# Kernel optimization log

Hardware: AMD Instinct MI355X
Metric: run time of the kernel (lower is better)

The kernel has to match this reference:

```python
import jax, jax.numpy as jnp
import numpy as np

B, L, D = 8, 4096, 1024
EPS = 1e-6


def setup_inputs() -> dict:
    key = jax.random.key(0)
    k1, k2, k3 = jax.random.split(key, 3)
    x = jax.random.normal(k1, (B, L, D), dtype=jnp.float32)
    # torch.nn.Linear default init ~ U(-1/sqrt(d), 1/sqrt(d)); scaled normal is fine for a reference
    w_in = jax.random.normal(k2, (3 * D, D), dtype=jnp.float32) * (D ** -0.5)
    w_out = jax.random.normal(k3, (D, D), dtype=jnp.float32) * (D ** -0.5)
    scale = jnp.ones((D,), dtype=jnp.float32)
    return {"x": x, "w_in": w_in, "w_out": w_out, "scale": scale}


def reference(x, w_in, w_out, scale):
    residual = x
    # RMSNorm: ||x||_2 * d^{-1/2}
    norm = jnp.linalg.norm(x, axis=-1, keepdims=True) * (x.shape[-1] ** -0.5)
    xn = scale * x / (norm + EPS)
    # proj_in: Linear(d, 3d, bias=False) -> chunk into g, v, f
    gvf = jnp.einsum('bld,ed->ble', xn, w_in)  # [B, L, 3D]
    g, v, f = jnp.split(gvf, 3, axis=-1)
    g = jax.nn.sigmoid(g)
    f = jax.nn.sigmoid(f - 1.0)

    # sequential gated linear recurrence: h_t = f_t * h_{t-1} + (1 - f_t) * v_t
    def step(h, fv):
        ft, vt = fv  # each [B, D]
        h = ft * h + (1.0 - ft) * vt
        return h, h

    h0 = jnp.zeros((x.shape[0], x.shape[2]), dtype=x.dtype)
    _, h_seq = jax.lax.scan(step, h0, (jnp.swapaxes(f, 0, 1), jnp.swapaxes(v, 0, 1)))
    h_seq = jnp.swapaxes(h_seq, 0, 1)  # [B, L, D]

    out = g * h_seq
    return residual + jnp.einsum('bld,ed->ble', out, w_out)
```

## Files before the change

kernel.cpp:

```cpp
#include <hip/hip_runtime.h>
#include <cstdint>
#include <cstddef>

typedef unsigned short u16;
typedef __attribute__((ext_vector_type(8))) short short8;
typedef __attribute__((ext_vector_type(4))) float floatx4;
typedef __attribute__((ext_vector_type(4))) unsigned short ushort4v;

constexpr int D_ = 1024;
constexpr int B_ = 8;
constexpr int L_ = 4096;
constexpr int M_ = B_ * L_;
constexpr int NCHUNK = 64;
constexpr int CLEN = L_ / NCHUNK;
constexpr float EPS_ = 1e-6f;
constexpr size_t WIN_ELEMS = (size_t)3 * D_ * D_;
constexpr size_t WOUT_ELEMS = (size_t)D_ * D_;
constexpr int NT_K = 16;

__device__ __forceinline__ float bf2f(u16 b) {
    union { unsigned u; float f; } x; x.u = ((unsigned)b) << 16; return x.f;
}
__device__ __forceinline__ u16 f2bf(float f) {
    union { float f; unsigned u; } x; x.f = f;
    unsigned r = x.u + 0x7fffu + ((x.u >> 16) & 1u);
    return (u16)(r >> 16);
}
__device__ __forceinline__ float sigmoidf_(float x) {
    return 1.f / (1.f + __expf(-x));
}
__device__ __forceinline__ short8 cvt8(const float* __restrict__ p) {
    float4 a = *(const float4*)p;
    float4 b = *(const float4*)(p + 4);
    short8 o;
    o[0] = (short)f2bf(a.x); o[1] = (short)f2bf(a.y);
    o[2] = (short)f2bf(a.z); o[3] = (short)f2bf(a.w);
    o[4] = (short)f2bf(b.x); o[5] = (short)f2bf(b.y);
    o[6] = (short)f2bf(b.z); o[7] = (short)f2bf(b.w);
    return o;
}
__device__ __forceinline__ void gload16(const void* g, void* l) {
    __builtin_amdgcn_global_load_lds((const __attribute__((address_space(1))) void*)g,
                                     (__attribute__((address_space(3))) void*)l, 16, 0, 0);
}

__global__ __launch_bounds__(256) void prep_xn_kernel(const float* __restrict__ x,
                                                      const float* __restrict__ scale,
                                                      u16* __restrict__ xn) {
    const int row = blockIdx.x;
    const int t = threadIdx.x;
    const float* xr = x + (size_t)row * D_;
    float4 xv = ((const float4*)xr)[t];
    float ss = xv.x * xv.x + xv.y * xv.y + xv.z * xv.z + xv.w * xv.w;
#pragma unroll
    for (int m = 32; m >= 1; m >>= 1) ss += __shfl_xor(ss, m, 64);
    __shared__ float red[4];
    const int wave = t >> 6, lane = t & 63;
    if (lane == 0) red[wave] = ss;
    __syncthreads();
    float tot = red[0] + red[1] + red[2] + red[3];
    float inv = 1.f / (sqrtf(tot * (1.f / D_)) + EPS_);
    float4 sv = ((const float4*)scale)[t];
    ushort4v o;
    o[0] = f2bf(xv.x * inv * sv.x);
    o[1] = f2bf(xv.y * inv * sv.y);
    o[2] = f2bf(xv.z * inv * sv.z);
    o[3] = f2bf(xv.w * inv * sv.w);
    ((ushort4v*)(xn + (size_t)row * D_))[t] = o;
}

__global__ __launch_bounds__(256) void prep_w_kernel(const float* __restrict__ w_in,
                                                     const float* __restrict__ w_out,
                                                     u16* __restrict__ w_in_bf,
                                                     u16* __restrict__ w_out_bf) {
    size_t i8 = ((size_t)blockIdx.x * 256 + threadIdx.x) * 8;
    if (i8 < WIN_ELEMS) {
        *(short8*)(w_in_bf + i8) = cvt8(w_in + i8);
    } else {
        size_t j = i8 - WIN_ELEMS;
        *(short8*)(w_out_bf + j) = cvt8(w_out + j);
    }
}


#define STAGE_A_(buf, half, koff) do { \
    const u16* g_ = gA0 + (koff) + (half) * 65536; \
    u16* l_ = (buf) + ((half) * 64 + iw) * 64; \
    gload16(g_, l_); gload16(g_ + 131072, l_ + 8192); } while (0)
#define STAGE_B_(buf, half, koff) do { \
    const u16* g_ = gB0 + (koff) + (half) * 32768; \
    u16* l_ = (buf) + (rBw + (half) * 32) * 64; \
    gload16(g_, l_); gload16(g_ + 131072, l_ + 8192); } while (0)
#define BARRIER_() do { __builtin_amdgcn_sched_barrier(0); \
    __builtin_amdgcn_s_barrier(); \
    __builtin_amdgcn_sched_barrier(0); } while (0)
#define LDA4_(mlo) do { \
    _Pragma("unroll") for (int m_ = 0; m_ < 4; ++m_) { \
      int o_ = aOff + ((mlo) + m_) * 2048; \
      af[m_][0] = *(const short8*)((const char*)curA + o_); \
      af[m_][1] = *(const short8*)((const char*)curA + (o_ ^ 64)); } } while (0)
#define LDB2_(nlo) do { \
    _Pragma("unroll") for (int n_ = 0; n_ < 2; ++n_) { \
      int o_ = bOff + ((nlo) + n_) * 2048; \
      bfv[n_][0] = *(const short8*)((const char*)curB + o_); \
      bfv[n_][1] = *(const short8*)((const char*)curB + (o_ ^ 64)); } } while (0)
#define MFMA_Q_(mlo, nlo) do { \
    __builtin_amdgcn_s_setprio(1); \
    _Pragma("unroll") for (int m_ = 0; m_ < 4; ++m_) \
    _Pragma("unroll") for (int n_ = 0; n_ < 2; ++n_) \
    _Pragma("unroll") for (int k_ = 0; k_ < 2; ++k_) \
      acc[(mlo) + m_][(nlo) + n_] = __builtin_amdgcn_mfma_f32_16x16x32_bf16( \
          af[m_][k_], bfv[n_][k_], acc[(mlo) + m_][(nlo) + n_], 0, 0, 0); \
    __builtin_amdgcn_s_setprio(0); } while (0)

__device__ __forceinline__ void tile_step(int tt, u16* curA, u16* curB, u16* othA, u16* othB,
                                          const u16* gA0, const u16* gB0, int iw, int rBw,
                                          int aOff, int bOff, floatx4 (&acc)[8][4]) {
    short8 af[4][2], bfv[2][2];
    const int k1 = (tt + 1) * 64, k2 = (tt + 2) * 64;
    const bool s1 = (tt + 1 < NT_K), s2 = (tt + 2 < NT_K);
    LDA4_(0); LDB2_(0);
    if (s1) STAGE_A_(othA, 1, k1);
    BARRIER_();
    MFMA_Q_(0, 0);
    BARRIER_();
    LDB2_(2);
    if (s1) STAGE_B_(othB, 1, k1);
    BARRIER_();
    MFMA_Q_(0, 2);
    BARRIER_();
    LDA4_(4); LDB2_(0);
    if (s2) STAGE_A_(curA, 0, k2);
    BARRIER_();
    MFMA_Q_(4, 0);
    BARRIER_();
    LDB2_(2);
    if (s2) STAGE_B_(curB, 0, k2);
    BARRIER_();
    MFMA_Q_(4, 2);
    if (s2)      { asm volatile("s_waitcnt vmcnt(4)" ::: "memory"); }
    else if (s1) { asm volatile("s_waitcnt vmcnt(0)" ::: "memory"); }
    BARRIER_();
}

__device__ __forceinline__ void gemm256_core(const u16* __restrict__ gA,
                                             const u16* __restrict__ gB,
                                             int m0, int n0,
                                             u16* __restrict__ As, u16* __restrict__ Bs,
                                             floatx4 (&acc)[8][4]) {
    const int t = threadIdx.x;
    const int wid = t >> 6, lane = t & 63;
    const int wr = wid >> 2, wc = wid & 3;
    const int l15 = lane & 15, quad = lane >> 4;
    const int jrow = lane >> 3, jc = lane & 7;
    const int swz = ((jc ^ (jrow & 7)) << 3);
    const u16* gA0 = gA + (size_t)(m0 + wid * 8 + jrow) * 1024 + swz;
    const int i0 = wid * 8 + jrow;
    const int rB0 = ((i0 >> 5) << 6) + (i0 & 31);
    const u16* gB0 = gB + (size_t)(n0 + rB0) * 1024 + swz;
    const int iw = wid * 8;
    const int rBw = ((iw >> 5) << 6) + (iw & 31);
    const int c0 = (quad * 16) ^ ((l15 & 7) << 4);
    const int aOff = (wr * 128 + l15) * 128 + c0;
    const int bOff = (wc * 64 + l15) * 128 + c0;

#pragma unroll
    for (int i = 0; i < 8; i++)
#pragma unroll
        for (int j = 0; j < 4; j++) { floatx4 z = {0.f, 0.f, 0.f, 0.f}; acc[i][j] = z; }

    STAGE_A_(As, 0, 0); STAGE_A_(As, 1, 0);
    STAGE_B_(Bs, 0, 0); STAGE_B_(Bs, 1, 0);
    STAGE_A_(As + 16384, 0, 64);
    STAGE_B_(Bs + 16384, 0, 64);
    asm volatile("s_waitcnt vmcnt(4)" ::: "memory");
    BARRIER_();

#pragma unroll 1
    for (int tt = 0; tt < NT_K; tt += 2) {
        tile_step(tt,     As,         Bs,         As + 16384, Bs + 16384,
                  gA0, gB0, iw, rBw, aOff, bOff, acc);
        tile_step(tt + 1, As + 16384, Bs + 16384, As,         Bs,
                  gA0, gB0, iw, rBw, aOff, bOff, acc);
    }
}

__global__ __launch_bounds__(512, 2) void gemm1_kernel(const u16* __restrict__ xn,
                                                       const u16* __restrict__ w_in,
                                                       u16* __restrict__ g_buf,
                                                       u16* __restrict__ v_buf,
                                                       u16* __restrict__ f_buf) {
    __shared__ __align__(16) u16 As[2 * 16384];
    __shared__ __align__(16) u16 Bs[2 * 16384];
    const int m0 = blockIdx.y * 256;
    const int n0 = blockIdx.x * 256;
    floatx4 acc[8][4];
    gemm256_core(xn, w_in, m0, n0, As, Bs, acc);

    const int t = threadIdx.x;
    const int wid = t >> 6, lane = t & 63;
    const int wr = wid >> 2, wc = wid & 3;
    const int l15 = lane & 15, quad = lane >> 4;
    const int plane = n0 >> 10;
    const int dcol0 = (n0 & 1023) + wc * 64;
    u16* dst = (plane == 0) ? g_buf : ((plane == 1) ? v_buf : f_buf);
    const int mrow0 = m0 + wr * 128 + quad * 4;
#pragma unroll
    for (int mt = 0; mt < 8; mt++) {
#pragma unroll
        for (int r = 0; r < 4; r++) {
            int m = mrow0 + mt * 16 + r;
#pragma unroll
            for (int nt = 0; nt < 4; nt++) {
                float val = acc[mt][nt][r];
                if (plane == 0) val = sigmoidf_(val);
                else if (plane == 2) val = sigmoidf_(val - 1.f);
                dst[(size_t)m * 1024 + dcol0 + nt * 16 + l15] = f2bf(val);
            }
        }
    }
}

__global__ __launch_bounds__(512, 2) void gemm2_kernel(const u16* __restrict__ op,
                                                       const u16* __restrict__ w_out,
                                                       const float* __restrict__ xres,
                                                       float* __restrict__ out) {
    __shared__ __align__(16) u16 As[2 * 16384];
    __shared__ __align__(16) u16 Bs[2 * 16384];
    const int m0 = blockIdx.y * 256;
    const int n0 = blockIdx.x * 256;
    floatx4 acc[8][4];
    gemm256_core(op, w_out, m0, n0, As, Bs, acc);

    const int t = threadIdx.x;
    const int wid = t >> 6, lane = t & 63;
    const int wr = wid >> 2, wc = wid & 3;
    const int l15 = lane & 15, quad = lane >> 4;
    const int ncol0 = n0 + wc * 64;
    const int mrow0 = m0 + wr * 128 + quad * 4;
#pragma unroll
    for (int mt = 0; mt < 8; mt++) {
#pragma unroll
        for (int r = 0; r < 4; r++) {
            int m = mrow0 + mt * 16 + r;
#pragma unroll
            for (int nt = 0; nt < 4; nt++) {
                size_t idx = (size_t)m * 1024 + ncol0 + nt * 16 + l15;
                out[idx] = acc[mt][nt][r] + xres[idx];
            }
        }
    }
}

__global__ __launch_bounds__(256) void scan1_kernel(const u16* __restrict__ f_buf,
                                                    const u16* __restrict__ v_buf,
                                                    float* __restrict__ Aarr,
                                                    float* __restrict__ Barr) {
    const int wid = blockIdx.x * 4 + (threadIdx.x >> 6);
    const int lane = threadIdx.x & 63;
    const int b = wid >> 10;
    const int rem = wid & 1023;
    const int c = rem >> 4;
    const int db = (rem & 15) * 64 + lane;
    float A = 1.f, Bv = 0.f;
    size_t base = ((size_t)b * L_ + c * CLEN) * D_ + db;
#pragma unroll 4
    for (int tt = 0; tt < CLEN; tt++) {
        float fv = bf2f(f_buf[base + (size_t)tt * D_]);
        float vv = bf2f(v_buf[base + (size_t)tt * D_]);
        A *= fv;
        Bv = fv * Bv + (1.f - fv) * vv;
    }
    size_t sidx = ((size_t)b * NCHUNK + c) * D_ + db;
    Aarr[sidx] = A;
    Barr[sidx] = Bv;
}

__global__ __launch_bounds__(256) void scan2_kernel(const float* __restrict__ Aarr,
                                                    const float* __restrict__ Barr,
                                                    float* __restrict__ hin) {
    const int id = blockIdx.x * 256 + threadIdx.x;
    const int b = id >> 10, d = id & 1023;
    float h = 0.f;
    for (int c = 0; c < NCHUNK; c++) {
        size_t idx = ((size_t)b * NCHUNK + c) * D_ + d;
        hin[idx] = h;
        h = Aarr[idx] * h + Barr[idx];
    }
}

__global__ __launch_bounds__(256) void scan3_kernel(const u16* __restrict__ f_buf,
                                                    const u16* __restrict__ v_buf,
                                                    u16* g_io,
                                                    const float* __restrict__ hin) {
    const int wid = blockIdx.x * 4 + (threadIdx.x >> 6);
    const int lane = threadIdx.x & 63;
    const int b = wid >> 10;
    const int rem = wid & 1023;
    const int c = rem >> 4;
    const int db = (rem & 15) * 64 + lane;
    size_t base = ((size_t)b * L_ + c * CLEN) * D_ + db;
    float h = hin[((size_t)b * NCHUNK + c) * D_ + db];
#pragma unroll 4
    for (int tt = 0; tt < CLEN; tt++) {
        size_t idx = base + (size_t)tt * D_;
        float fv = bf2f(f_buf[idx]);
        float vv = bf2f(v_buf[idx]);
        float gv = bf2f(g_io[idx]);
        h = fv * h + (1.f - fv) * vv;
        g_io[idx] = f2bf(gv * h);
    }
}

extern "C" void kernel_launch(void* const* d_in, const int* in_sizes, int n_in,
                              void* d_out, int out_size, void* d_ws, size_t ws_size,
                              hipStream_t stream) {
    const float* x     = (const float*)d_in[0];
    const float* w_in  = (const float*)d_in[1];
    const float* w_out = (const float*)d_in[2];
    const float* scale = (const float*)d_in[3];
    float* out = (float*)d_out;

    u16* f_buf = (u16*)d_out;
    u16* v_buf = (u16*)d_out + (size_t)M_ * D_;

    char* ws = (char*)d_ws;
    const size_t PLANE = (size_t)M_ * D_ * sizeof(u16);
    u16* xn    = (u16*)ws;
    u16* g_buf = (u16*)(ws + PLANE);
    u16* w_in_bf  = (u16*)(ws + 2 * PLANE);
    u16* w_out_bf = w_in_bf + WIN_ELEMS;
    float* Aarr = (float*)(ws + 2 * PLANE + (WIN_ELEMS + WOUT_ELEMS) * sizeof(u16));
    float* Barr = Aarr + (size_t)B_ * NCHUNK * D_;
    float* hin  = Barr + (size_t)B_ * NCHUNK * D_;

    prep_xn_kernel<<<M_, 256, 0, stream>>>(x, scale, xn);
    prep_w_kernel<<<(int)((WIN_ELEMS + WOUT_ELEMS) / 8 / 256), 256, 0, stream>>>(
        w_in, w_out, w_in_bf, w_out_bf);
    gemm1_kernel<<<dim3(3 * D_ / 256, M_ / 256), 512, 0, stream>>>(
        xn, w_in_bf, g_buf, v_buf, f_buf);
    scan1_kernel<<<(B_ * NCHUNK * 16) / 4, 256, 0, stream>>>(f_buf, v_buf, Aarr, Barr);
    scan2_kernel<<<(B_ * D_) / 256, 256, 0, stream>>>(Aarr, Barr, hin);
    scan3_kernel<<<(B_ * NCHUNK * 16) / 4, 256, 0, stream>>>(f_buf, v_buf, g_buf, hin);
    gemm2_kernel<<<dim3(D_ / 256, M_ / 256), 512, 0, stream>>>(g_buf, w_out_bf, x, out);
}
```

Measured before the change: 638.1 us.

## Fuse prep kernels, remap GEMM tiles per XCD, stage gemm1 epilogue through LDS

```diff
diff --git a/kernel.cpp b/kernel.cpp
--- a/kernel.cpp
+++ b/kernel.cpp
@@ -17,6 +17,7 @@
 constexpr size_t WIN_ELEMS = (size_t)3 * D_ * D_;
 constexpr size_t WOUT_ELEMS = (size_t)D_ * D_;
 constexpr int NT_K = 16;
+constexpr int PREPW_BLOCKS = (int)((WIN_ELEMS + WOUT_ELEMS) / 8 / 256);
 
 __device__ __forceinline__ float bf2f(u16 b) {
     union { unsigned u; float f; } x; x.u = ((unsigned)b) << 16; return x.f;
@@ -44,11 +45,25 @@
                                      (__attribute__((address_space(3))) void*)l, 16, 0, 0);
 }
 
-__global__ __launch_bounds__(256) void prep_xn_kernel(const float* __restrict__ x,
-                                                      const float* __restrict__ scale,
-                                                      u16* __restrict__ xn) {
+__global__ __launch_bounds__(256) void prep_kernel(const float* __restrict__ x,
+                                                   const float* __restrict__ scale,
+                                                   u16* __restrict__ xn,
+                                                   const float* __restrict__ w_in,
+                                                   const float* __restrict__ w_out,
+                                                   u16* __restrict__ w_in_bf,
+                                                   u16* __restrict__ w_out_bf) {
+    const int t = threadIdx.x;
+    if ((int)blockIdx.x >= M_) {
+        size_t i8 = ((size_t)(blockIdx.x - M_) * 256 + t) * 8;
+        if (i8 < WIN_ELEMS) {
+            *(short8*)(w_in_bf + i8) = cvt8(w_in + i8);
+        } else {
+            size_t j = i8 - WIN_ELEMS;
+            *(short8*)(w_out_bf + j) = cvt8(w_out + j);
+        }
+        return;
+    }
     const int row = blockIdx.x;
-    const int t = threadIdx.x;
     const float* xr = x + (size_t)row * D_;
     float4 xv = ((const float4*)xr)[t];
     float ss = xv.x * xv.x + xv.y * xv.y + xv.z * xv.z + xv.w * xv.w;
@@ -67,19 +82,6 @@
     o[2] = f2bf(xv.z * inv * sv.z);
     o[3] = f2bf(xv.w * inv * sv.w);
     ((ushort4v*)(xn + (size_t)row * D_))[t] = o;
-}
-
-__global__ __launch_bounds__(256) void prep_w_kernel(const float* __restrict__ w_in,
-                                                     const float* __restrict__ w_out,
-                                                     u16* __restrict__ w_in_bf,
-                                                     u16* __restrict__ w_out_bf) {
-    size_t i8 = ((size_t)blockIdx.x * 256 + threadIdx.x) * 8;
-    if (i8 < WIN_ELEMS) {
-        *(short8*)(w_in_bf + i8) = cvt8(w_in + i8);
-    } else {
-        size_t j = i8 - WIN_ELEMS;
-        *(short8*)(w_out_bf + j) = cvt8(w_out + j);
-    }
 }
 
 
@@ -185,39 +187,56 @@
     }
 }
 
+__device__ __forceinline__ void xcd_decode(int nwg, int& m0, int& n0) {
+    int lid = blockIdx.x;
+    int cid = (lid & 7) * (nwg >> 3) + (lid >> 3);
+    m0 = (cid & 127) << 8;
+    n0 = (cid >> 7) << 8;
+}
+
 __global__ __launch_bounds__(512, 2) void gemm1_kernel(const u16* __restrict__ xn,
                                                        const u16* __restrict__ w_in,
                                                        u16* __restrict__ g_buf,
                                                        u16* __restrict__ v_buf,
                                                        u16* __restrict__ f_buf) {
-    __shared__ __align__(16) u16 As[2 * 16384];
-    __shared__ __align__(16) u16 Bs[2 * 16384];
-    const int m0 = blockIdx.y * 256;
-    const int n0 = blockIdx.x * 256;
+    __shared__ __align__(16) u16 SH[65536];
+    int m0, n0;
+    xcd_decode(1536, m0, n0);
     floatx4 acc[8][4];
-    gemm256_core(xn, w_in, m0, n0, As, Bs, acc);
+    gemm256_core(xn, w_in, m0, n0, SH, SH + 32768, acc);
 
     const int t = threadIdx.x;
     const int wid = t >> 6, lane = t & 63;
     const int wr = wid >> 2, wc = wid & 3;
     const int l15 = lane & 15, quad = lane >> 4;
     const int plane = n0 >> 10;
-    const int dcol0 = (n0 & 1023) + wc * 64;
+    const int cbase = n0 & 1023;
     u16* dst = (plane == 0) ? g_buf : ((plane == 1) ? v_buf : f_buf);
-    const int mrow0 = m0 + wr * 128 + quad * 4;
+
 #pragma unroll
     for (int mt = 0; mt < 8; mt++) {
 #pragma unroll
         for (int r = 0; r < 4; r++) {
-            int m = mrow0 + mt * 16 + r;
+            int row = wr * 128 + mt * 16 + quad * 4 + r;
+            int xr = (row & 7) << 3;
 #pragma unroll
             for (int nt = 0; nt < 4; nt++) {
+                int colb = (wc * 64 + nt * 16 + l15) * 2;
                 float val = acc[mt][nt][r];
                 if (plane == 0) val = sigmoidf_(val);
                 else if (plane == 2) val = sigmoidf_(val - 1.f);
-                dst[(size_t)m * 1024 + dcol0 + nt * 16 + l15] = f2bf(val);
+                *(u16*)((char*)SH + row * 512 + (colb ^ xr)) = f2bf(val);
             }
         }
+    }
+    __syncthreads();
+    const int lane8 = lane * 8;
+#pragma unroll 4
+    for (int i = 0; i < 32; i++) {
+        int row = wid + i * 8;
+        int xr = (row & 7) << 3;
+        uint2 v = *(const uint2*)((const char*)SH + row * 512 + (lane8 ^ xr));
+        *(uint2*)(dst + (size_t)(m0 + row) * 1024 + cbase + lane * 4) = v;
     }
 }
 
@@ -225,12 +244,11 @@
                                                        const u16* __restrict__ w_out,
                                                        const float* __restrict__ xres,
                                                        float* __restrict__ out) {
-    __shared__ __align__(16) u16 As[2 * 16384];
-    __shared__ __align__(16) u16 Bs[2 * 16384];
-    const int m0 = blockIdx.y * 256;
-    const int n0 = blockIdx.x * 256;
+    __shared__ __align__(16) u16 SH[65536];
+    int m0, n0;
+    xcd_decode(512, m0, n0);
     floatx4 acc[8][4];
-    gemm256_core(op, w_out, m0, n0, As, Bs, acc);
+    gemm256_core(op, w_out, m0, n0, SH, SH + 32768, acc);
 
     const int t = threadIdx.x;
     const int wid = t >> 6, lane = t & 63;
@@ -334,13 +352,11 @@
     float* Barr = Aarr + (size_t)B_ * NCHUNK * D_;
     float* hin  = Barr + (size_t)B_ * NCHUNK * D_;
 
-    prep_xn_kernel<<<M_, 256, 0, stream>>>(x, scale, xn);
-    prep_w_kernel<<<(int)((WIN_ELEMS + WOUT_ELEMS) / 8 / 256), 256, 0, stream>>>(
-        w_in, w_out, w_in_bf, w_out_bf);
-    gemm1_kernel<<<dim3(3 * D_ / 256, M_ / 256), 512, 0, stream>>>(
-        xn, w_in_bf, g_buf, v_buf, f_buf);
+    prep_kernel<<<M_ + PREPW_BLOCKS, 256, 0, stream>>>(x, scale, xn, w_in, w_out,
+                                                       w_in_bf, w_out_bf);
+    gemm1_kernel<<<1536, 512, 0, stream>>>(xn, w_in_bf, g_buf, v_buf, f_buf);
     scan1_kernel<<<(B_ * NCHUNK * 16) / 4, 256, 0, stream>>>(f_buf, v_buf, Aarr, Barr);
     scan2_kernel<<<(B_ * D_) / 256, 256, 0, stream>>>(Aarr, Barr, hin);
     scan3_kernel<<<(B_ * NCHUNK * 16) / 4, 256, 0, stream>>>(f_buf, v_buf, g_buf, hin);
-    gemm2_kernel<<<dim3(D_ / 256, M_ / 256), 512, 0, stream>>>(g_buf, w_out_bf, x, out);
-}
+    gemm2_kernel<<<512, 512, 0, stream>>>(g_buf, w_out_bf, x, out);
+}
```

New measurement: 662.8 us. +3.9%, slower.
